# Kernel tuning notes

Measured on AMD Instinct MI355X. Metric: run time of the kernel, lower is better.

Reference implementation:

```python
import jax, jax.numpy as jnp
import numpy as np

# ---- Kymatio-style Morlet scattering filter bank (J=2, L=8, padded 40x40) ----
_CACHE = {}
_MP = 40  # 32 + 2*4 reflect padding, as in kymatio compute_padding for J=2

def _gabor(M, N, sigma, theta, xi, slant):
    R = np.array([[np.cos(theta), -np.sin(theta)], [np.sin(theta), np.cos(theta)]])
    D = np.array([[1.0, 0.0], [0.0, slant ** 2]])
    curv = R @ D @ R.T / (2.0 * sigma ** 2)
    xx, yy = np.mgrid[0:M, 0:N]
    gab = np.zeros((M, N), np.complex128)
    for ex in range(-2, 3):  # periodize over 5x5 shifts
        for ey in range(-2, 3):
            xg = xx + ex * M
            yg = yy + ey * N
            arg = -(curv[0, 0] * xg * xg + (curv[0, 1] + curv[1, 0]) * xg * yg + curv[1, 1] * yg * yg) \
                  + 1j * (xg * xi * np.cos(theta) + yg * xi * np.sin(theta))
            gab += np.exp(arg)
    return gab / (2.0 * np.pi * sigma ** 2 / slant)

def _morlet(M, N, sigma, theta, xi, slant):
    wv = _gabor(M, N, sigma, theta, xi, slant)
    env = _gabor(M, N, sigma, theta, 0.0, slant)
    return wv - (wv.sum() / env.sum()) * env  # zero-mean Morlet

def _periodize(v, res):
    k = 2 ** res
    Mv, Nv = v.shape
    return v.reshape(k, Mv // k, k, Nv // k).mean(axis=(0, 2))

def _filters():
    if _CACHE:
        return _CACHE
    Mp = _MP
    phi = np.real(np.fft.fft2(_gabor(Mp, Mp, 0.8 * 2 ** 2, 0.0, 0.0, 1.0)))
    psis = {}
    for j in range(2):
        bank = []
        for t in range(8):
            theta = (3 - t) * np.pi / 8.0  # kymatio angle convention (L=8)
            bank.append(np.real(np.fft.fft2(_morlet(Mp, Mp, 0.8 * 2 ** j, theta, 3.0 * np.pi / 4.0 / 2 ** j, 0.5))))
        psis[j] = np.stack(bank)
    _CACHE['phi0'] = jnp.asarray(phi, jnp.float32)
    _CACHE['phi1'] = jnp.asarray(_periodize(phi, 1), jnp.float32)
    _CACHE['psi0'] = jnp.asarray(psis[0], jnp.float32)      # (8,40,40) j=0 at res 0
    _CACHE['psi1_r0'] = jnp.asarray(psis[1], jnp.float32)   # (8,40,40) j=1 at res 0
    return _CACHE

def _unpad_sub(y_real, k):
    # fourier lowpass output -> spatial subsample by k, then unpad 1-pixel border
    return y_real[..., ::k, ::k][..., 1:-1, 1:-1]

def _scatter(x):
    F = _filters()
    xp = jnp.pad(x, ((0, 0), (0, 0), (4, 4), (4, 4)), mode='reflect')  # (B,3,40,40)
    xf = jnp.fft.fft2(xp)
    def lowpass(u, phi, k):
        return _unpad_sub(jnp.fft.ifft2(jnp.fft.fft2(u) * phi).real, k)
    # order 0
    S0 = _unpad_sub(jnp.fft.ifft2(xf * F['phi0']).real, 4)[:, :, None]            # (B,3,1,8,8)
    # order 1, j1 = 0 (stays at res 0)
    U1a = jnp.abs(jnp.fft.ifft2(xf[:, :, None] * F['psi0']))                       # (B,3,8,40,40)
    S1a = lowpass(U1a, F['phi0'], 4)                                               # (B,3,8,8,8)
    # order 1, j1 = 1 (subsample by 2)
    U1b = jnp.abs(jnp.fft.ifft2(xf[:, :, None] * F['psi1_r0'])[..., ::2, ::2])     # (B,3,8,20,20)
    S1b = lowpass(U1b, F['phi1'], 2)                                               # (B,3,8,8,8)
    # order 2, j1=0 -> j2=1
    U2 = jnp.abs(jnp.fft.ifft2(jnp.fft.fft2(U1a)[:, :, :, None] * F['psi1_r0'])[..., ::2, ::2])  # (B,3,8,8,20,20)
    S2 = lowpass(U2, F['phi1'], 2).reshape(x.shape[0], 3, 64, 8, 8)
    return jnp.concatenate([S0, S1a, S1b, S2], axis=2)  # (B,3,81,8,8)

def _toeplitz_mult(G, H, v):
    # ToeplitzLike, corner=False -> f=(0,0): y = sum_i L(g_i) (L(h_i)^T v)
    # L(.) lower-triangular Toeplitz; done via length-2n FFT conv / correlation
    n = v.shape[-1]
    Lf = 2 * n
    Hf = jnp.fft.rfft(H, Lf)          # (r, F)
    Gf = jnp.fft.rfft(G, Lf)          # (r, F)
    Vf = jnp.fft.rfft(v, Lf)          # (B, F)
    T = jnp.fft.irfft(jnp.conj(Hf)[:, None, :] * Vf[None], Lf)[..., :n]   # (r,B,n) = L(h_i)^T v
    Tf = jnp.fft.rfft(T, Lf)
    y = jnp.fft.irfft(jnp.einsum('rf,rbf->bf', Gf, Tf), Lf)[..., :n]       # sum_i L(g_i) t_i
    return y

def setup_inputs() -> dict:
    key = jax.random.key(0)
    ks = jax.random.split(key, 5)
    B, n, r = 128, 3 * 81 * 8 * 8, 4
    x = jax.random.normal(ks[0], (B, 3, 32, 32), jnp.float32)
    gamma = jnp.ones((n,), jnp.float32)
    beta = jnp.zeros((n,), jnp.float32)
    G = jax.random.normal(ks[3], (r, n), jnp.float32) / np.float32(np.sqrt(n))
    H = jax.random.normal(ks[4], (r, n), jnp.float32) / np.float32(np.sqrt(n))
    return {"x": x, "gamma": gamma, "beta": beta, "G": G, "H": H}

def reference(x, gamma, beta, G, H):
    S = _scatter(x)                                   # (B,3,81,8,8)
    f = S.reshape(S.shape[0], -1)                     # (B, 15552)
    mu = f.mean(axis=0)
    var = f.var(axis=0)                               # biased var, training-mode BN
    f = (f - mu) / jnp.sqrt(var + 1e-5) * gamma + beta
    f = jax.nn.relu(f)
    y = _toeplitz_mult(G, H, f)
    return y[..., :10]
```

## Files before the change

kernel.cpp:

```cpp
#include <hip/hip_runtime.h>
#include <math.h>

#define NTHR 256

__device__ __forceinline__ int reflect32(int v) {
  if (v < 0) v = -v;
  if (v > 31) v = 62 - v;
  return v;
}

__device__ __forceinline__ void init_tw(float2* tw, int N, int tid) {
  for (int j = tid; j < N; j += NTHR) {
    float s, c;
    sincosf(-2.0f * (float)M_PI * (float)j / (float)N, &s, &c);
    tw[j] = make_float2(c, s);
  }
}

template<int N, int LD, int NK, bool INV, int B, int AS>
__device__ __forceinline__ void dftB_rows(const float2* __restrict__ io,
                                          float2* __restrict__ tmp,
                                          const float2* __restrict__ tw, int tid) {
  constexpr int G = N / NK;
  constexpr int UNITS = B * N * G;
  for (int u = tid; u < UNITS; u += NTHR) {
    const int a = u / (N * G);
    const int rem = u - a * (N * G);
    const int r = rem / G, kg = rem - G * r;
    float xr[NK], xi[NK], ar[NK], ai[NK];
#pragma unroll
    for (int j = 0; j < NK; ++j) {
      float2 w = tw[kg * NK + j];
      xr[j] = w.x; xi[j] = INV ? -w.y : w.y;
    }
    const float2* row = io + a * AS + r * LD;
    float2 v = row[N - 1];
#pragma unroll
    for (int j = 0; j < NK; ++j) { ar[j] = v.x; ai[j] = v.y; }
#pragma unroll 2
    for (int cc = N - 2; cc >= 0; --cc) {
      v = row[cc];
#pragma unroll
      for (int j = 0; j < NK; ++j) {
        float nr = fmaf(ar[j], xr[j], fmaf(-ai[j], xi[j], v.x));
        float ni = fmaf(ar[j], xi[j], fmaf(ai[j], xr[j], v.y));
        ar[j] = nr; ai[j] = ni;
      }
    }
    float2* orow = tmp + a * AS + r * LD + kg * NK;
#pragma unroll
    for (int j = 0; j < NK; ++j) orow[j] = make_float2(ar[j], ai[j]);
  }
}

template<int N, int LD, int NK, bool INV, int B, int AS>
__device__ __forceinline__ void dftB_cols(const float2* __restrict__ tmp,
                                          float2* __restrict__ io,
                                          const float2* __restrict__ tw, int tid) {
  constexpr int G = N / NK;
  constexpr int UNITS = B * N * G;
  for (int u = tid; u < UNITS; u += NTHR) {
    const int a = u / (N * G);
    const int rem = u - a * (N * G);
    const int k1g = rem / N, k2 = rem - N * k1g;
    float xr[NK], xi[NK], ar[NK], ai[NK];
#pragma unroll
    for (int j = 0; j < NK; ++j) {
      float2 w = tw[k1g * NK + j];
      xr[j] = w.x; xi[j] = INV ? -w.y : w.y;
    }
    const float2* col = tmp + a * AS + k2;
    float2 v = col[(N - 1) * LD];
#pragma unroll
    for (int j = 0; j < NK; ++j) { ar[j] = v.x; ai[j] = v.y; }
#pragma unroll 2
    for (int r = N - 2; r >= 0; --r) {
      v = col[r * LD];
#pragma unroll
      for (int j = 0; j < NK; ++j) {
        float nr = fmaf(ar[j], xr[j], fmaf(-ai[j], xi[j], v.x));
        float ni = fmaf(ar[j], xi[j], fmaf(ai[j], xr[j], v.y));
        ar[j] = nr; ai[j] = ni;
      }
    }
    constexpr float scale = INV ? (1.f / (float)(N * N)) : 1.f;
#pragma unroll
    for (int j = 0; j < NK; ++j)
      io[a * AS + (k1g * NK + j) * LD + k2] = make_float2(ar[j] * scale, ai[j] * scale);
  }
}

template<int N, int LD, int NK, bool INV, int B, int AS>
__device__ __forceinline__ void dft2dB(float2* io, float2* tmp, const float2* tw, int tid) {
  dftB_rows<N, LD, NK, INV, B, AS>(io, tmp, tw, tid);
  __syncthreads();
  dftB_cols<N, LD, NK, INV, B, AS>(tmp, io, tw, tid);
  __syncthreads();
}

template<int NK, int KH>
__device__ __forceinline__ void rdft40_rows(const float2* __restrict__ io,
                                            float2* __restrict__ tmp,
                                            const float2* __restrict__ tw, int tid) {
  constexpr int G = KH / NK;
  constexpr int UNITS = 40 * G;
  if (tid < UNITS) {
    const int r = tid / G, kg = tid - G * r;
    float xr[NK], xi[NK], ar[NK], ai[NK];
#pragma unroll
    for (int j = 0; j < NK; ++j) { float2 w = tw[kg * NK + j]; xr[j] = w.x; xi[j] = w.y; }
    const float2* row = io + r * 41;
    float v = row[39].x;
#pragma unroll
    for (int j = 0; j < NK; ++j) { ar[j] = v; ai[j] = 0.f; }
#pragma unroll 2
    for (int cc = 38; cc >= 0; --cc) {
      v = row[cc].x;
#pragma unroll
      for (int j = 0; j < NK; ++j) {
        float nr = fmaf(ar[j], xr[j], fmaf(-ai[j], xi[j], v));
        float ni = fmaf(ar[j], xi[j], ai[j] * xr[j]);
        ar[j] = nr; ai[j] = ni;
      }
    }
    float2* orow = tmp + r * 41 + kg * NK;
#pragma unroll
    for (int j = 0; j < NK; ++j) orow[j] = make_float2(ar[j], ai[j]);
  }
}

template<int NK, int KH>
__device__ __forceinline__ void dft40_colsK(const float2* __restrict__ tmp,
                                            float2* __restrict__ io,
                                            const float2* __restrict__ tw, int tid) {
  constexpr int G = 40 / NK;
  constexpr int UNITS = KH * G;
  if (tid < UNITS) {
    const int k1g = tid / KH, k2 = tid - KH * k1g;
    float xr[NK], xi[NK], ar[NK], ai[NK];
#pragma unroll
    for (int j = 0; j < NK; ++j) { float2 w = tw[k1g * NK + j]; xr[j] = w.x; xi[j] = w.y; }
    const float2* col = tmp + k2;
    float2 v = col[39 * 41];
#pragma unroll
    for (int j = 0; j < NK; ++j) { ar[j] = v.x; ai[j] = v.y; }
#pragma unroll 2
    for (int r = 38; r >= 0; --r) {
      v = col[r * 41];
#pragma unroll
      for (int j = 0; j < NK; ++j) {
        float nr = fmaf(ar[j], xr[j], fmaf(-ai[j], xi[j], v.x));
        float ni = fmaf(ar[j], xi[j], fmaf(ai[j], xr[j], v.y));
        ar[j] = nr; ai[j] = ni;
      }
    }
#pragma unroll
    for (int j = 0; j < NK; ++j)
      io[(k1g * NK + j) * 41 + k2] = make_float2(ar[j], ai[j]);
  }
}

__device__ __forceinline__ void mirror40(float2* __restrict__ A, int tid) {
  for (int o = tid; o < 760; o += NTHR) {
    int d = o / 40;
    int k2 = 21 + d, k1 = o - 40 * d;
    float2 v = A[((40 - k1) % 40) * 41 + (40 - k2)];
    A[k1 * 41 + k2] = make_float2(v.x, -v.y);
  }
}

__global__ __launch_bounds__(NTHR) void k_filters(float* __restrict__ filt) {
  const int fid = blockIdx.x;
  const int tid = threadIdx.x;

  __shared__ float2 WV[40 * 41];
  __shared__ float  EV[1600];
  __shared__ float2 T[40 * 41];
  __shared__ float2 tw40[40];
  __shared__ float  sred[3][4];
  __shared__ float  Kc[2];

  double sigma, theta, xi, slant; int morlet; int outOff;
  if (fid == 0)      { sigma = 3.2; theta = 0.0; xi = 0.0;                  slant = 1.0; morlet = 0; outOff = 0; }
  else if (fid <= 8) { int t = fid - 1; sigma = 0.8; theta = (3 - t) * M_PI / 8.0; xi = 3.0 * M_PI / 4.0; slant = 0.5; morlet = 1; outOff = 2000 + t * 1600; }
  else               { int t = fid - 9; sigma = 1.6; theta = (3 - t) * M_PI / 8.0; xi = 3.0 * M_PI / 8.0; slant = 0.5; morlet = 1; outOff = 14800 + t * 1600; }

  const double ctd = cos(theta), std_ = sin(theta);
  const double sl2 = slant * slant;
  const double inv2s = 1.0 / (2.0 * sigma * sigma);
  const float ca = (float)((ctd * ctd + sl2 * std_ * std_) * inv2s);
  const float cb = (float)((ctd * std_ * (1.0 - sl2)) * inv2s);
  const float cd = (float)((std_ * std_ + sl2 * ctd * ctd) * inv2s);
  const float rnorm = (float)(slant / (2.0 * M_PI * sigma * sigma));
  const float ct = (float)ctd, st = (float)std_;
  const float xif = (float)xi;

  float swr = 0.f, swi = 0.f, ser = 0.f;
  for (int o = tid; o < 1600; o += NTHR) {
    int xr = o / 40, yc = o - 40 * xr;
    float wr = 0.f, wi = 0.f, er = 0.f;
    for (int ex = -2; ex <= 2; ++ex) {
      for (int ey = -2; ey <= 2; ++ey) {
        float xg = (float)xr + ex * 40.f, yg = (float)yc + ey * 40.f;
        float e = expf(-(ca * xg * xg + 2.f * cb * xg * yg + cd * yg * yg));
        float ang = xif * (xg * ct + yg * st);
        float s, c;
        sincosf(ang, &s, &c);
        wr = fmaf(e, c, wr); wi = fmaf(e, s, wi); er += e;
      }
    }
    wr *= rnorm; wi *= rnorm; er *= rnorm;
    WV[xr * 41 + yc] = make_float2(wr, wi);
    EV[o] = er;
    swr += wr; swi += wi; ser += er;
  }
  for (int off = 32; off > 0; off >>= 1) {
    swr += __shfl_down(swr, off);
    swi += __shfl_down(swi, off);
    ser += __shfl_down(ser, off);
  }
  int lane = tid & 63, w = tid >> 6;
  if (lane == 0) { sred[0][w] = swr; sred[1][w] = swi; sred[2][w] = ser; }
  __syncthreads();
  if (tid == 0) {
    float A = 0, B = 0, C = 0;
    for (int i = 0; i < 4; ++i) { A += sred[0][i]; B += sred[1][i]; C += sred[2][i]; }
    Kc[0] = A / C; Kc[1] = B / C;
  }
  init_tw(tw40, 40, tid);
  __syncthreads();
  if (morlet) {
    for (int o = tid; o < 1600; o += NTHR) {
      int i = o / 40, j = o - 40 * i;
      float e = EV[o];
      WV[i * 41 + j].x -= Kc[0] * e;
      WV[i * 41 + j].y -= Kc[1] * e;
    }
  }
  __syncthreads();
  dft2dB<40, 41, 8, false, 1, 0>(WV, T, tw40, tid);
  for (int o = tid; o < 1600; o += NTHR) {
    int i = o / 40, j = o - 40 * i;
    filt[outOff + o] = WV[i * 41 + j].x;
  }
  if (fid == 0) {
    for (int q = tid; q < 400; q += NTHR) {
      int q1 = q / 20, q2 = q - 20 * q1;
      float v = 0.25f * (WV[q1 * 41 + q2].x + WV[(q1 + 20) * 41 + q2].x +
                         WV[q1 * 41 + (q2 + 20)].x + WV[(q1 + 20) * 41 + (q2 + 20)].x);
      filt[1600 + q] = v;
    }
  }
}

__global__ __launch_bounds__(NTHR) void k_fftx(const float* __restrict__ x,
                                               const float* __restrict__ filt,
                                               float2* __restrict__ xf_g,
                                               float* __restrict__ f) {
  const int bc = blockIdx.x;
  const int b = bc / 3, c = bc - 3 * b;
  const int tid = threadIdx.x;

  __shared__ float2 A[40 * 41], T[40 * 41];
  __shared__ float2 P[110], Q[110];
  __shared__ float2 tw40[40], tw10[10];

  init_tw(tw40, 40, tid);
  init_tw(tw10, 10, tid);

  const float* xb = x + (size_t)bc * 1024;
  for (int o = tid; o < 1600; o += NTHR) {
    int i = o / 40, j = o - 40 * i;
    int si = reflect32(i - 4), sj = reflect32(j - 4);
    A[i * 41 + j] = make_float2(xb[si * 32 + sj], 0.f);
  }
  __syncthreads();
  rdft40_rows<4, 24>(A, T, tw40, tid);
  __syncthreads();
  dft40_colsK<4, 24>(T, A, tw40, tid);
  __syncthreads();
  mirror40(A, tid);
  __syncthreads();
  for (int o = tid; o < 1600; o += NTHR) {
    int i = o / 40, j = o - 40 * i;
    xf_g[(size_t)bc * 1600 + o] = A[i * 41 + j];
  }

  const float* phi0 = filt;
  for (int q = tid; q < 100; q += NTHR) {
    int q1 = q / 10, q2 = q - 10 * q1;
    float re = 0.f, im = 0.f;
#pragma unroll
    for (int a2 = 0; a2 < 4; ++a2)
#pragma unroll
      for (int b2 = 0; b2 < 4; ++b2) {
        int i40 = q1 + 10 * a2, j40 = q2 + 10 * b2;
        float ph = phi0[i40 * 40 + j40];
        float2 v = A[i40 * 41 + j40];
        re = fmaf(v.x, ph, re); im = fmaf(v.y, ph, im);
      }
    P[q1 * 11 + q2] = make_float2(re * (1.f / 16.f), im * (1.f / 16.f));
  }
  __syncthreads();
  dft2dB<10, 11, 1, true, 1, 0>(P, Q, tw10, tid);
  float* fb = f + (size_t)b * 15552 + c * 5184;
  if (tid < 64) {
    int i = tid >> 3, j = tid & 7;
    fb[tid] = P[(i + 1) * 11 + (j + 1)].x;
  }
}

__global__ __launch_bounds__(NTHR) void k_main(const float2* __restrict__ xf_g,
                                               const float* __restrict__ filt,
                                               float* __restrict__ f) {
  const int blk = blockIdx.x;
  const int t = blk & 7;
  const int bc = blk >> 3;
  const int b = bc / 3, c = bc - 3 * b;
  const int tid = threadIdx.x;

  __shared__ float2 A[40 * 41];
  __shared__ float2 T[40 * 41];
  __shared__ float2 C[2 * 420];
  __shared__ float2 P[110], Q[110];
  __shared__ float2 tw40[40], tw20[20], tw10[10];

  const float* phi0 = filt;
  const float* phi1 = filt + 1600;
  const float* psi0 = filt + 2000;
  const float* psi1 = filt + 14800;

  init_tw(tw40, 40, tid);
  init_tw(tw20, 20, tid);
  init_tw(tw10, 10, tid);

  const float2* xf = xf_g + (size_t)bc * 1600;
  for (int o = tid; o < 1600; o += NTHR) {
    int i = o / 40, j = o - 40 * i;
    A[i * 41 + j] = xf[o];
  }
  __syncthreads();

  float* fb = f + (size_t)b * 15552 + c * 5184;

  const float* ps1t = psi1 + t * 1600;
  for (int q = tid; q < 400; q += NTHR) {
    int q1 = q / 20, q2 = q - 20 * q1;
    float re = 0.f, im = 0.f;
#pragma unroll
    for (int a2 = 0; a2 < 2; ++a2)
#pragma unroll
      for (int b2 = 0; b2 < 2; ++b2) {
        int i40 = q1 + 20 * a2, j40 = q2 + 20 * b2;
        float ph = ps1t[i40 * 40 + j40];
        float2 v = A[i40 * 41 + j40];
        re = fmaf(v.x, ph, re); im = fmaf(v.y, ph, im);
      }
    C[q1 * 21 + q2] = make_float2(re * 0.25f, im * 0.25f);
  }
  __syncthreads();
  dft2dB<20, 21, 2, true, 1, 420>(C, T, tw20, tid);
  for (int o = tid; o < 400; o += NTHR) {
    int i = o / 20, j = o - 20 * i;
    float2 z = C[i * 21 + j];
    C[i * 21 + j] = make_float2(sqrtf(fmaf(z.x, z.x, z.y * z.y)), 0.f);
  }
  __syncthreads();
  dft2dB<20, 21, 2, false, 1, 420>(C, T, tw20, tid);
  for (int q = tid; q < 100; q += NTHR) {
    int q1 = q / 10, q2 = q - 10 * q1;
    float re = 0.f, im = 0.f;
#pragma unroll
    for (int a2 = 0; a2 < 2; ++a2)
#pragma unroll
      for (int b2 = 0; b2 < 2; ++b2) {
        int i20 = q1 + 10 * a2, j20 = q2 + 10 * b2;
        float ph = phi1[i20 * 20 + j20];
        float2 v = C[i20 * 21 + j20];
        re = fmaf(v.x, ph, re); im = fmaf(v.y, ph, im);
      }
    Q[q1 * 11 + q2] = make_float2(re * 0.25f, im * 0.25f);
  }

  const float* ps0 = psi0 + t * 1600;
  for (int o = tid; o < 1600; o += NTHR) {
    int i = o / 40, j = o - 40 * i;
    float p = ps0[o];
    float2 v = A[i * 41 + j];
    A[i * 41 + j] = make_float2(v.x * p, v.y * p);
  }
  __syncthreads();
  dft2dB<40, 41, 8, true, 1, 0>(A, T, tw40, tid);
  for (int o = tid; o < 1600; o += NTHR) {
    int i = o / 40, j = o - 40 * i;
    float2 z = A[i * 41 + j];
    A[i * 41 + j] = make_float2(sqrtf(fmaf(z.x, z.x, z.y * z.y)), 0.f);
  }
  __syncthreads();
  rdft40_rows<4, 24>(A, T, tw40, tid);
  __syncthreads();
  dft40_colsK<4, 24>(T, A, tw40, tid);
  __syncthreads();
  mirror40(A, tid);
  __syncthreads();

  for (int q = tid; q < 100; q += NTHR) {
    int q1 = q / 10, q2 = q - 10 * q1;
    float re = 0.f, im = 0.f;
#pragma unroll
    for (int a2 = 0; a2 < 4; ++a2)
#pragma unroll
      for (int b2 = 0; b2 < 4; ++b2) {
        int i40 = q1 + 10 * a2, j40 = q2 + 10 * b2;
        float ph = phi0[i40 * 40 + j40];
        float2 v = A[i40 * 41 + j40];
        re = fmaf(v.x, ph, re); im = fmaf(v.y, ph, im);
      }
    float2 qb = Q[q1 * 11 + q2];
    P[q1 * 11 + q2] = make_float2(re * (1.f / 16.f) - qb.y, im * (1.f / 16.f) + qb.x);
  }
  __syncthreads();
  dft2dB<10, 11, 1, true, 1, 0>(P, C, tw10, tid);
  if (tid < 64) {
    int i = tid >> 3, j = tid & 7;
    float2 v = P[(i + 1) * 11 + (j + 1)];
    fb[(1 + t) * 64 + tid] = v.x;
    fb[(9 + t) * 64 + tid] = v.y;
  }

  for (int p = 0; p < 4; ++p) {
    const float* pa = psi1 + (2 * p) * 1600;
    const float* pb = psi1 + (2 * p + 1) * 1600;
    __syncthreads();
    for (int q = tid; q < 800; q += NTHR) {
      int a = (q >= 400) ? 1 : 0;
      int qq = q - 400 * a;
      const float* ps = a ? pb : pa;
      int q1 = qq / 20, q2 = qq - 20 * q1;
      float re = 0.f, im = 0.f;
#pragma unroll
      for (int a2 = 0; a2 < 2; ++a2)
#pragma unroll
        for (int b2 = 0; b2 < 2; ++b2) {
          int i40 = q1 + 20 * a2, j40 = q2 + 20 * b2;
          float ph = ps[i40 * 40 + j40];
          float2 v = A[i40 * 41 + j40];
          re = fmaf(v.x, ph, re); im = fmaf(v.y, ph, im);
        }
      C[a * 420 + q1 * 21 + q2] = make_float2(re * 0.25f, im * 0.25f);
    }
    __syncthreads();
    dft2dB<20, 21, 2, true, 2, 420>(C, T, tw20, tid);
    for (int o = tid; o < 400; o += NTHR) {
      int i = o / 20, j = o - 20 * i;
      int idx = i * 21 + j;
      float2 z0 = C[idx], z1 = C[420 + idx];
      C[idx] = make_float2(sqrtf(fmaf(z0.x, z0.x, z0.y * z0.y)),
                           sqrtf(fmaf(z1.x, z1.x, z1.y * z1.y)));
    }
    __syncthreads();
    dft2dB<20, 21, 2, false, 1, 420>(C, T, tw20, tid);
    for (int q = tid; q < 100; q += NTHR) {
      int q1 = q / 10, q2 = q - 10 * q1;
      float re = 0.f, im = 0.f;
#pragma unroll
      for (int a2 = 0; a2 < 2; ++a2)
#pragma unroll
        for (int b2 = 0; b2 < 2; ++b2) {
          int i20 = q1 + 10 * a2, j20 = q2 + 10 * b2;
          float ph = phi1[i20 * 20 + j20];
          float2 v = C[i20 * 21 + j20];
          re = fmaf(v.x, ph, re); im = fmaf(v.y, ph, im);
        }
      P[q1 * 11 + q2] = make_float2(re * 0.25f, im * 0.25f);
    }
    __syncthreads();
    dft2dB<10, 11, 1, true, 1, 0>(P, C + 420, tw10, tid);
    if (tid < 64) {
      int i = tid >> 3, j = tid & 7;
      float2 v = P[(i + 1) * 11 + (j + 1)];
      fb[(17 + t * 8 + 2 * p) * 64 + tid] = v.x;
      fb[(17 + t * 8 + 2 * p + 1) * 64 + tid] = v.y;
    }
  }
}

__global__ __launch_bounds__(NTHR) void k_bn(const float* __restrict__ f,
                                             float* __restrict__ mu,
                                             float* __restrict__ rstd) {
  int col = blockIdx.x * NTHR + threadIdx.x;
  if (col >= 15552) return;
  double s = 0.0, s2 = 0.0;
  for (int b = 0; b < 128; ++b) {
    float v = f[(size_t)b * 15552 + col];
    s += v; s2 += (double)v * v;
  }
  double m = s / 128.0;
  double var = s2 / 128.0 - m * m;
  mu[col] = (float)m;
  rstd[col] = (float)(1.0 / sqrt(var + 1e-5));
}

__global__ __launch_bounds__(NTHR) void k_norm(const float* __restrict__ f,
                                               const float* __restrict__ mu,
                                               const float* __restrict__ rstd,
                                               const float* __restrict__ gamma,
                                               const float* __restrict__ beta,
                                               float* __restrict__ g) {
  size_t i = (size_t)blockIdx.x * NTHR + threadIdx.x;
  if (i >= (size_t)128 * 15552) return;
  int col = (int)(i % 15552);
  float v = (f[i] - mu[col]) * rstd[col] * gamma[col] + beta[col];
  g[i] = v > 0.f ? v : 0.f;
}

__global__ __launch_bounds__(NTHR) void k_out(const float* __restrict__ g,
                                              const float* __restrict__ Gm,
                                              const float* __restrict__ Hm,
                                              float* __restrict__ out) {
  const int b = blockIdx.x;
  const int tid = threadIdx.x;
  const float* gb = g + (size_t)b * 15552;

  float acc[40];
#pragma unroll
  for (int i = 0; i < 40; ++i) acc[i] = 0.f;

  for (int j = tid; j < 15552; j += NTHR) {
    float h[4];
#pragma unroll
    for (int r = 0; r < 4; ++r) h[r] = Hm[r * 15552 + j];
#pragma unroll
    for (int m = 0; m < 10; ++m) {
      int jm = j + m;
      float gv = (jm < 15552) ? gb[jm] : 0.f;
#pragma unroll
      for (int r = 0; r < 4; ++r) acc[r * 10 + m] += h[r] * gv;
    }
  }
#pragma unroll
  for (int i = 0; i < 40; ++i)
    for (int off = 32; off > 0; off >>= 1)
      acc[i] += __shfl_down(acc[i], off);

  __shared__ float red[4][40];
  __shared__ float Tm[40];
  int lane = tid & 63, w = tid >> 6;
  if (lane == 0) {
#pragma unroll
    for (int i = 0; i < 40; ++i) red[w][i] = acc[i];
  }
  __syncthreads();
  if (tid < 40) Tm[tid] = red[0][tid] + red[1][tid] + red[2][tid] + red[3][tid];
  __syncthreads();
  if (tid < 10) {
    float y = 0.f;
    for (int r = 0; r < 4; ++r)
      for (int m = 0; m <= tid; ++m)
        y += Gm[r * 15552 + (tid - m)] * Tm[r * 10 + m];
    out[b * 10 + tid] = y;
  }
}

extern "C" void kernel_launch(void* const* d_in, const int* in_sizes, int n_in,
                              void* d_out, int out_size, void* d_ws, size_t ws_size,
                              hipStream_t stream) {
  (void)in_sizes; (void)n_in; (void)out_size; (void)ws_size;
  const float* x     = (const float*)d_in[0];
  const float* gamma = (const float*)d_in[1];
  const float* beta  = (const float*)d_in[2];
  const float* G     = (const float*)d_in[3];
  const float* H     = (const float*)d_in[4];
  float* out = (float*)d_out;

  float* ws   = (float*)d_ws;
  float* filt = ws;
  float* xf   = filt + 27600;
  float* f    = xf + 1228800;
  float* g    = f + 1990656;
  float* mu   = g + 1990656;
  float* rstd = mu + 15552;

  k_filters<<<17, NTHR, 0, stream>>>(filt);
  k_fftx<<<384, NTHR, 0, stream>>>(x, filt, (float2*)xf, f);
  k_main<<<3072, NTHR, 0, stream>>>((const float2*)xf, filt, f);
  k_bn<<<61, NTHR, 0, stream>>>(f, mu, rstd);
  k_norm<<<7776, NTHR, 0, stream>>>(f, mu, rstd, gamma, beta, g);
  k_out<<<128, NTHR, 0, stream>>>(g, G, H, out);
}
```

Measured before the change: 393.3 us.

## Use radix-8x5 FFT for 40-point transforms, pre-permute filters, fuse BN into output

Replaces the direct 40-point DFTs (real-input rows plus mirror) with a two-stage 8x5 Cooley-Tukey factorisation with twiddles. This cuts the per-image FFT arithmetic in the main and input kernels. The filter kernel now stores lowpass filters pre-scaled and permuted so the periodization sums can use float4 loads. The four second-order inverse 10x10 transforms are batched into one pass, and the phi1 lowpass result is folded directly into the combined P buffer. The normalize+ReLU kernel is fused into the Toeplitz output kernel via a shared-memory tile, removing the intermediate g buffer and one launch.

```diff
diff --git a/kernel.cpp b/kernel.cpp
--- a/kernel.cpp
+++ b/kernel.cpp
@@ -98,75 +98,150 @@
   __syncthreads();
 }
 
-template<int NK, int KH>
-__device__ __forceinline__ void rdft40_rows(const float2* __restrict__ io,
-                                            float2* __restrict__ tmp,
-                                            const float2* __restrict__ tw, int tid) {
-  constexpr int G = KH / NK;
-  constexpr int UNITS = 40 * G;
-  if (tid < UNITS) {
-    const int r = tid / G, kg = tid - G * r;
-    float xr[NK], xi[NK], ar[NK], ai[NK];
-#pragma unroll
-    for (int j = 0; j < NK; ++j) { float2 w = tw[kg * NK + j]; xr[j] = w.x; xi[j] = w.y; }
-    const float2* row = io + r * 41;
-    float v = row[39].x;
-#pragma unroll
-    for (int j = 0; j < NK; ++j) { ar[j] = v; ai[j] = 0.f; }
-#pragma unroll 2
-    for (int cc = 38; cc >= 0; --cc) {
-      v = row[cc].x;
-#pragma unroll
-      for (int j = 0; j < NK; ++j) {
-        float nr = fmaf(ar[j], xr[j], fmaf(-ai[j], xi[j], v));
-        float ni = fmaf(ar[j], xi[j], ai[j] * xr[j]);
-        ar[j] = nr; ai[j] = ni;
-      }
-    }
-    float2* orow = tmp + r * 41 + kg * NK;
-#pragma unroll
-    for (int j = 0; j < NK; ++j) orow[j] = make_float2(ar[j], ai[j]);
-  }
-}
-
-template<int NK, int KH>
-__device__ __forceinline__ void dft40_colsK(const float2* __restrict__ tmp,
-                                            float2* __restrict__ io,
-                                            const float2* __restrict__ tw, int tid) {
-  constexpr int G = 40 / NK;
-  constexpr int UNITS = KH * G;
-  if (tid < UNITS) {
-    const int k1g = tid / KH, k2 = tid - KH * k1g;
-    float xr[NK], xi[NK], ar[NK], ai[NK];
-#pragma unroll
-    for (int j = 0; j < NK; ++j) { float2 w = tw[k1g * NK + j]; xr[j] = w.x; xi[j] = w.y; }
-    const float2* col = tmp + k2;
-    float2 v = col[39 * 41];
-#pragma unroll
-    for (int j = 0; j < NK; ++j) { ar[j] = v.x; ai[j] = v.y; }
-#pragma unroll 2
-    for (int r = 38; r >= 0; --r) {
-      v = col[r * 41];
-#pragma unroll
-      for (int j = 0; j < NK; ++j) {
-        float nr = fmaf(ar[j], xr[j], fmaf(-ai[j], xi[j], v.x));
-        float ni = fmaf(ar[j], xi[j], fmaf(ai[j], xr[j], v.y));
-        ar[j] = nr; ai[j] = ni;
-      }
-    }
-#pragma unroll
-    for (int j = 0; j < NK; ++j)
-      io[(k1g * NK + j) * 41 + k2] = make_float2(ar[j], ai[j]);
-  }
-}
-
-__device__ __forceinline__ void mirror40(float2* __restrict__ A, int tid) {
-  for (int o = tid; o < 760; o += NTHR) {
-    int d = o / 40;
-    int k2 = 21 + d, k1 = o - 40 * d;
-    float2 v = A[((40 - k1) % 40) * 41 + (40 - k2)];
-    A[k1 * 41 + k2] = make_float2(v.x, -v.y);
-  }
+template<bool INV>
+__device__ __forceinline__ void r40_rowsA(const float2* __restrict__ io, float2* __restrict__ T,
+                                          const float2* __restrict__ tw, int tid) {
+  if (tid < 200) {
+    const int r = tid / 5, n2 = tid - 5 * r;
+    const float2* base = io + r * 41 + n2;
+    float xr[8], xi[8], ar[8], ai[8];
+#pragma unroll
+    for (int k1 = 0; k1 < 8; ++k1) {
+      float2 w = tw[5 * k1];
+      xr[k1] = w.x; xi[k1] = INV ? -w.y : w.y;
+    }
+    float2 v = base[35];
+#pragma unroll
+    for (int k1 = 0; k1 < 8; ++k1) { ar[k1] = v.x; ai[k1] = v.y; }
+#pragma unroll
+    for (int n1 = 6; n1 >= 0; --n1) {
+      v = base[5 * n1];
+#pragma unroll
+      for (int k1 = 0; k1 < 8; ++k1) {
+        float nr = fmaf(ar[k1], xr[k1], fmaf(-ai[k1], xi[k1], v.x));
+        float ni = fmaf(ar[k1], xi[k1], fmaf(ai[k1], xr[k1], v.y));
+        ar[k1] = nr; ai[k1] = ni;
+      }
+    }
+    float2* o = T + r * 41 + n2 * 8;
+#pragma unroll
+    for (int k1 = 0; k1 < 8; ++k1) {
+      float2 w = tw[n2 * k1];
+      float wy = INV ? -w.y : w.y;
+      o[k1] = make_float2(ar[k1] * w.x - ai[k1] * wy, ar[k1] * wy + ai[k1] * w.x);
+    }
+  }
+}
+
+template<bool INV>
+__device__ __forceinline__ void r40_rowsB(const float2* __restrict__ T, float2* __restrict__ io,
+                                          const float2* __restrict__ tw, int tid) {
+  for (int u = tid; u < 320; u += NTHR) {
+    const int r = u >> 3, k1 = u & 7;
+    const float2* base = T + r * 41 + k1;
+    float xr[5], xi[5], ar[5], ai[5];
+#pragma unroll
+    for (int k2 = 0; k2 < 5; ++k2) {
+      float2 w = tw[8 * k2];
+      xr[k2] = w.x; xi[k2] = INV ? -w.y : w.y;
+    }
+    float2 v = base[32];
+#pragma unroll
+    for (int k2 = 0; k2 < 5; ++k2) { ar[k2] = v.x; ai[k2] = v.y; }
+#pragma unroll
+    for (int n2 = 3; n2 >= 0; --n2) {
+      v = base[n2 * 8];
+#pragma unroll
+      for (int k2 = 0; k2 < 5; ++k2) {
+        float nr = fmaf(ar[k2], xr[k2], fmaf(-ai[k2], xi[k2], v.x));
+        float ni = fmaf(ar[k2], xi[k2], fmaf(ai[k2], xr[k2], v.y));
+        ar[k2] = nr; ai[k2] = ni;
+      }
+    }
+    float2* o = io + r * 41 + k1;
+#pragma unroll
+    for (int k2 = 0; k2 < 5; ++k2) o[8 * k2] = make_float2(ar[k2], ai[k2]);
+  }
+}
+
+template<bool INV>
+__device__ __forceinline__ void r40_colsA(const float2* __restrict__ io, float2* __restrict__ T,
+                                          const float2* __restrict__ tw, int tid) {
+  if (tid < 200) {
+    const int n2 = tid / 40, c = tid - 40 * n2;
+    const float2* base = io + n2 * 41 + c;
+    float xr[8], xi[8], ar[8], ai[8];
+#pragma unroll
+    for (int k1 = 0; k1 < 8; ++k1) {
+      float2 w = tw[5 * k1];
+      xr[k1] = w.x; xi[k1] = INV ? -w.y : w.y;
+    }
+    float2 v = base[35 * 41];
+#pragma unroll
+    for (int k1 = 0; k1 < 8; ++k1) { ar[k1] = v.x; ai[k1] = v.y; }
+#pragma unroll
+    for (int n1 = 6; n1 >= 0; --n1) {
+      v = base[5 * n1 * 41];
+#pragma unroll
+      for (int k1 = 0; k1 < 8; ++k1) {
+        float nr = fmaf(ar[k1], xr[k1], fmaf(-ai[k1], xi[k1], v.x));
+        float ni = fmaf(ar[k1], xi[k1], fmaf(ai[k1], xr[k1], v.y));
+        ar[k1] = nr; ai[k1] = ni;
+      }
+    }
+    float2* o = T + n2 * 8 * 41 + c;
+#pragma unroll
+    for (int k1 = 0; k1 < 8; ++k1) {
+      float2 w = tw[n2 * k1];
+      float wy = INV ? -w.y : w.y;
+      o[k1 * 41] = make_float2(ar[k1] * w.x - ai[k1] * wy, ar[k1] * wy + ai[k1] * w.x);
+    }
+  }
+}
+
+template<bool INV>
+__device__ __forceinline__ void r40_colsB(const float2* __restrict__ T, float2* __restrict__ io,
+                                          const float2* __restrict__ tw, int tid) {
+  constexpr float scale = INV ? (1.f / 1600.f) : 1.f;
+  for (int u = tid; u < 320; u += NTHR) {
+    const int k1 = u / 40, c = u - 40 * k1;
+    const float2* base = T + k1 * 41 + c;
+    float xr[5], xi[5], ar[5], ai[5];
+#pragma unroll
+    for (int k2 = 0; k2 < 5; ++k2) {
+      float2 w = tw[8 * k2];
+      xr[k2] = w.x; xi[k2] = INV ? -w.y : w.y;
+    }
+    float2 v = base[4 * 8 * 41];
+#pragma unroll
+    for (int k2 = 0; k2 < 5; ++k2) { ar[k2] = v.x; ai[k2] = v.y; }
+#pragma unroll
+    for (int n2 = 3; n2 >= 0; --n2) {
+      v = base[n2 * 8 * 41];
+#pragma unroll
+      for (int k2 = 0; k2 < 5; ++k2) {
+        float nr = fmaf(ar[k2], xr[k2], fmaf(-ai[k2], xi[k2], v.x));
+        float ni = fmaf(ar[k2], xi[k2], fmaf(ai[k2], xr[k2], v.y));
+        ar[k2] = nr; ai[k2] = ni;
+      }
+    }
+    float2* o = io + k1 * 41 + c;
+#pragma unroll
+    for (int k2 = 0; k2 < 5; ++k2)
+      o[8 * k2 * 41] = make_float2(ar[k2] * scale, ai[k2] * scale);
+  }
+}
+
+template<bool INV>
+__device__ __forceinline__ void radix40(float2* io, float2* T, const float2* tw, int tid) {
+  r40_rowsA<INV>(io, T, tw, tid);
+  __syncthreads();
+  r40_rowsB<INV>(T, io, tw, tid);
+  __syncthreads();
+  r40_colsA<INV>(io, T, tw, tid);
+  __syncthreads();
+  r40_colsB<INV>(T, io, tw, tid);
+  __syncthreads();
 }
 
 __global__ __launch_bounds__(NTHR) void k_filters(float* __restrict__ filt) {
@@ -180,10 +255,10 @@
   __shared__ float  sred[3][4];
   __shared__ float  Kc[2];
 
-  double sigma, theta, xi, slant; int morlet; int outOff;
-  if (fid == 0)      { sigma = 3.2; theta = 0.0; xi = 0.0;                  slant = 1.0; morlet = 0; outOff = 0; }
-  else if (fid <= 8) { int t = fid - 1; sigma = 0.8; theta = (3 - t) * M_PI / 8.0; xi = 3.0 * M_PI / 4.0; slant = 0.5; morlet = 1; outOff = 2000 + t * 1600; }
-  else               { int t = fid - 9; sigma = 1.6; theta = (3 - t) * M_PI / 8.0; xi = 3.0 * M_PI / 8.0; slant = 0.5; morlet = 1; outOff = 14800 + t * 1600; }
+  double sigma, theta, xi, slant; int morlet;
+  if (fid == 0)      { sigma = 3.2; theta = 0.0; xi = 0.0;                  slant = 1.0; morlet = 0; }
+  else if (fid <= 8) { int t = fid - 1; sigma = 0.8; theta = (3 - t) * M_PI / 8.0; xi = 3.0 * M_PI / 4.0; slant = 0.5; morlet = 1; }
+  else               { int t = fid - 9; sigma = 1.6; theta = (3 - t) * M_PI / 8.0; xi = 3.0 * M_PI / 8.0; slant = 0.5; morlet = 1; }
 
   const double ctd = cos(theta), std_ = sin(theta);
   const double sl2 = slant * slant;
@@ -239,16 +314,42 @@
   }
   __syncthreads();
   dft2dB<40, 41, 8, false, 1, 0>(WV, T, tw40, tid);
-  for (int o = tid; o < 1600; o += NTHR) {
-    int i = o / 40, j = o - 40 * i;
-    filt[outOff + o] = WV[i * 41 + j].x;
-  }
+
   if (fid == 0) {
+    for (int o = tid; o < 1600; o += NTHR) {
+      int q = o >> 4, j = o & 15;
+      int q1 = q / 10, q2 = q - 10 * q1;
+      int a2 = j >> 2, b2 = j & 3;
+      filt[o] = WV[(q1 + 10 * a2) * 41 + (q2 + 10 * b2)].x * (1.f / 16.f);
+    }
+    for (int m = tid; m < 400; m += NTHR) {
+      int m1 = m / 20, m2 = m - 20 * m1;
+      EV[m] = 0.25f * (WV[m1 * 41 + m2].x + WV[(m1 + 20) * 41 + m2].x +
+                       WV[m1 * 41 + m2 + 20].x + WV[(m1 + 20) * 41 + m2 + 20].x);
+    }
+    __syncthreads();
+    for (int o = tid; o < 400; o += NTHR) {
+      int q = o >> 2, j = o & 3;
+      int q1 = q / 10, q2 = q - 10 * q1;
+      int a2 = j >> 1, b2 = j & 1;
+      filt[1600 + o] = EV[(q1 + 10 * a2) * 20 + (q2 + 10 * b2)] * 0.25f;
+    }
+  } else if (fid <= 8) {
+    int t = fid - 1;
+    for (int o = tid; o < 1600; o += NTHR) {
+      int i = o / 40, j = o - 40 * i;
+      filt[2000 + t * 1600 + o] = WV[i * 41 + j].x;
+    }
+  } else {
+    int t = fid - 9;
     for (int q = tid; q < 400; q += NTHR) {
       int q1 = q / 20, q2 = q - 20 * q1;
-      float v = 0.25f * (WV[q1 * 41 + q2].x + WV[(q1 + 20) * 41 + q2].x +
-                         WV[q1 * 41 + (q2 + 20)].x + WV[(q1 + 20) * 41 + (q2 + 20)].x);
-      filt[1600 + q] = v;
+      int base = q1 * 41 + q2;
+      float* o = filt + 14800 + t * 1600 + q * 4;
+      o[0] = WV[base].x * 0.25f;
+      o[1] = WV[base + 20].x * 0.25f;
+      o[2] = WV[base + 820].x * 0.25f;
+      o[3] = WV[base + 840].x * 0.25f;
     }
   }
 }
@@ -262,7 +363,7 @@
   const int tid = threadIdx.x;
 
   __shared__ float2 A[40 * 41], T[40 * 41];
-  __shared__ float2 P[110], Q[110];
+  __shared__ float2 P[110];
   __shared__ float2 tw40[40], tw10[10];
 
   init_tw(tw40, 40, tid);
@@ -275,34 +376,31 @@
     A[i * 41 + j] = make_float2(xb[si * 32 + sj], 0.f);
   }
   __syncthreads();
-  rdft40_rows<4, 24>(A, T, tw40, tid);
-  __syncthreads();
-  dft40_colsK<4, 24>(T, A, tw40, tid);
-  __syncthreads();
-  mirror40(A, tid);
-  __syncthreads();
+  radix40<false>(A, T, tw40, tid);
   for (int o = tid; o < 1600; o += NTHR) {
     int i = o / 40, j = o - 40 * i;
     xf_g[(size_t)bc * 1600 + o] = A[i * 41 + j];
   }
 
-  const float* phi0 = filt;
+  const float4* ph0f4 = (const float4*)filt;
   for (int q = tid; q < 100; q += NTHR) {
     int q1 = q / 10, q2 = q - 10 * q1;
+    int base = q1 * 41 + q2;
     float re = 0.f, im = 0.f;
 #pragma unroll
-    for (int a2 = 0; a2 < 4; ++a2)
-#pragma unroll
-      for (int b2 = 0; b2 < 4; ++b2) {
-        int i40 = q1 + 10 * a2, j40 = q2 + 10 * b2;
-        float ph = phi0[i40 * 40 + j40];
-        float2 v = A[i40 * 41 + j40];
-        re = fmaf(v.x, ph, re); im = fmaf(v.y, ph, im);
-      }
-    P[q1 * 11 + q2] = make_float2(re * (1.f / 16.f), im * (1.f / 16.f));
-  }
-  __syncthreads();
-  dft2dB<10, 11, 1, true, 1, 0>(P, Q, tw10, tid);
+    for (int a2 = 0; a2 < 4; ++a2) {
+      float4 pf = ph0f4[q * 4 + a2];
+      float2 v0 = A[base + a2 * 410];
+      float2 v1 = A[base + a2 * 410 + 10];
+      float2 v2 = A[base + a2 * 410 + 20];
+      float2 v3 = A[base + a2 * 410 + 30];
+      re = fmaf(v0.x, pf.x, fmaf(v1.x, pf.y, fmaf(v2.x, pf.z, fmaf(v3.x, pf.w, re))));
+      im = fmaf(v0.y, pf.x, fmaf(v1.y, pf.y, fmaf(v2.y, pf.z, fmaf(v3.y, pf.w, im))));
+    }
+    P[q1 * 11 + q2] = make_float2(re, im);
+  }
+  __syncthreads();
+  dft2dB<10, 11, 1, true, 1, 0>(P, T, tw10, tid);
   float* fb = f + (size_t)b * 15552 + c * 5184;
   if (tid < 64) {
     int i = tid >> 3, j = tid & 7;
@@ -322,13 +420,14 @@
   __shared__ float2 A[40 * 41];
   __shared__ float2 T[40 * 41];
   __shared__ float2 C[2 * 420];
-  __shared__ float2 P[110], Q[110];
+  __shared__ float2 P[110];
+  __shared__ float2 P4[4 * 110];
   __shared__ float2 tw40[40], tw20[20], tw10[10];
 
-  const float* phi0 = filt;
-  const float* phi1 = filt + 1600;
-  const float* psi0 = filt + 2000;
-  const float* psi1 = filt + 14800;
+  const float4* ph0f4 = (const float4*)filt;
+  const float4* ph1f4 = (const float4*)(filt + 1600);
+  const float*  psi0  = filt + 2000;
+  const float4* ps1f4 = (const float4*)(filt + 14800);
 
   init_tw(tw40, 40, tid);
   init_tw(tw20, 20, tid);
@@ -343,20 +442,14 @@
 
   float* fb = f + (size_t)b * 15552 + c * 5184;
 
-  const float* ps1t = psi1 + t * 1600;
   for (int q = tid; q < 400; q += NTHR) {
     int q1 = q / 20, q2 = q - 20 * q1;
-    float re = 0.f, im = 0.f;
-#pragma unroll
-    for (int a2 = 0; a2 < 2; ++a2)
-#pragma unroll
-      for (int b2 = 0; b2 < 2; ++b2) {
-        int i40 = q1 + 20 * a2, j40 = q2 + 20 * b2;
-        float ph = ps1t[i40 * 40 + j40];
-        float2 v = A[i40 * 41 + j40];
-        re = fmaf(v.x, ph, re); im = fmaf(v.y, ph, im);
-      }
-    C[q1 * 21 + q2] = make_float2(re * 0.25f, im * 0.25f);
+    int base = q1 * 41 + q2;
+    float4 pf = ps1f4[t * 400 + q];
+    float2 v0 = A[base], v1 = A[base + 20], v2 = A[base + 820], v3 = A[base + 840];
+    float re = fmaf(v0.x, pf.x, fmaf(v1.x, pf.y, fmaf(v2.x, pf.z, v3.x * pf.w)));
+    float im = fmaf(v0.y, pf.x, fmaf(v1.y, pf.y, fmaf(v2.y, pf.z, v3.y * pf.w)));
+    C[q1 * 21 + q2] = make_float2(re, im);
   }
   __syncthreads();
   dft2dB<20, 21, 2, true, 1, 420>(C, T, tw20, tid);
@@ -369,20 +462,16 @@
   dft2dB<20, 21, 2, false, 1, 420>(C, T, tw20, tid);
   for (int q = tid; q < 100; q += NTHR) {
     int q1 = q / 10, q2 = q - 10 * q1;
-    float re = 0.f, im = 0.f;
-#pragma unroll
-    for (int a2 = 0; a2 < 2; ++a2)
-#pragma unroll
-      for (int b2 = 0; b2 < 2; ++b2) {
-        int i20 = q1 + 10 * a2, j20 = q2 + 10 * b2;
-        float ph = phi1[i20 * 20 + j20];
-        float2 v = C[i20 * 21 + j20];
-        re = fmaf(v.x, ph, re); im = fmaf(v.y, ph, im);
-      }
-    Q[q1 * 11 + q2] = make_float2(re * 0.25f, im * 0.25f);
+    int base = q1 * 21 + q2;
+    float4 pf = ph1f4[q];
+    float2 v0 = C[base], v1 = C[base + 10], v2 = C[base + 210], v3 = C[base + 220];
+    float re = fmaf(v0.x, pf.x, fmaf(v1.x, pf.y, fmaf(v2.x, pf.z, v3.x * pf.w)));
+    float im = fmaf(v0.y, pf.x, fmaf(v1.y, pf.y, fmaf(v2.y, pf.z, v3.y * pf.w)));
+    P[q1 * 11 + q2] = make_float2(-im, re);
   }
 
   const float* ps0 = psi0 + t * 1600;
+  __syncthreads();
   for (int o = tid; o < 1600; o += NTHR) {
     int i = o / 40, j = o - 40 * i;
     float p = ps0[o];
@@ -390,37 +479,34 @@
     A[i * 41 + j] = make_float2(v.x * p, v.y * p);
   }
   __syncthreads();
-  dft2dB<40, 41, 8, true, 1, 0>(A, T, tw40, tid);
+  radix40<true>(A, T, tw40, tid);
   for (int o = tid; o < 1600; o += NTHR) {
     int i = o / 40, j = o - 40 * i;
     float2 z = A[i * 41 + j];
     A[i * 41 + j] = make_float2(sqrtf(fmaf(z.x, z.x, z.y * z.y)), 0.f);
   }
   __syncthreads();
-  rdft40_rows<4, 24>(A, T, tw40, tid);
-  __syncthreads();
-  dft40_colsK<4, 24>(T, A, tw40, tid);
-  __syncthreads();
-  mirror40(A, tid);
-  __syncthreads();
+  radix40<false>(A, T, tw40, tid);
 
   for (int q = tid; q < 100; q += NTHR) {
     int q1 = q / 10, q2 = q - 10 * q1;
+    int base = q1 * 41 + q2;
     float re = 0.f, im = 0.f;
 #pragma unroll
-    for (int a2 = 0; a2 < 4; ++a2)
-#pragma unroll
-      for (int b2 = 0; b2 < 4; ++b2) {
-        int i40 = q1 + 10 * a2, j40 = q2 + 10 * b2;
-        float ph = phi0[i40 * 40 + j40];
-        float2 v = A[i40 * 41 + j40];
-        re = fmaf(v.x, ph, re); im = fmaf(v.y, ph, im);
-      }
-    float2 qb = Q[q1 * 11 + q2];
-    P[q1 * 11 + q2] = make_float2(re * (1.f / 16.f) - qb.y, im * (1.f / 16.f) + qb.x);
-  }
-  __syncthreads();
-  dft2dB<10, 11, 1, true, 1, 0>(P, C, tw10, tid);
+    for (int a2 = 0; a2 < 4; ++a2) {
+      float4 pf = ph0f4[q * 4 + a2];
+      float2 v0 = A[base + a2 * 410];
+      float2 v1 = A[base + a2 * 410 + 10];
+      float2 v2 = A[base + a2 * 410 + 20];
+      float2 v3 = A[base + a2 * 410 + 30];
+      re = fmaf(v0.x, pf.x, fmaf(v1.x, pf.y, fmaf(v2.x, pf.z, fmaf(v3.x, pf.w, re))));
+      im = fmaf(v0.y, pf.x, fmaf(v1.y, pf.y, fmaf(v2.y, pf.z, fmaf(v3.y, pf.w, im))));
+    }
+    float2 prev = P[q1 * 11 + q2];
+    P[q1 * 11 + q2] = make_float2(prev.x + re, prev.y + im);
+  }
+  __syncthreads();
+  dft2dB<10, 11, 1, true, 1, 0>(P, T, tw10, tid);
   if (tid < 64) {
     int i = tid >> 3, j = tid & 7;
     float2 v = P[(i + 1) * 11 + (j + 1)];
@@ -429,25 +515,17 @@
   }
 
   for (int p = 0; p < 4; ++p) {
-    const float* pa = psi1 + (2 * p) * 1600;
-    const float* pb = psi1 + (2 * p + 1) * 1600;
     __syncthreads();
-    for (int q = tid; q < 800; q += NTHR) {
-      int a = (q >= 400) ? 1 : 0;
-      int qq = q - 400 * a;
-      const float* ps = a ? pb : pa;
-      int q1 = qq / 20, q2 = qq - 20 * q1;
-      float re = 0.f, im = 0.f;
-#pragma unroll
-      for (int a2 = 0; a2 < 2; ++a2)
-#pragma unroll
-        for (int b2 = 0; b2 < 2; ++b2) {
-          int i40 = q1 + 20 * a2, j40 = q2 + 20 * b2;
-          float ph = ps[i40 * 40 + j40];
-          float2 v = A[i40 * 41 + j40];
-          re = fmaf(v.x, ph, re); im = fmaf(v.y, ph, im);
-        }
-      C[a * 420 + q1 * 21 + q2] = make_float2(re * 0.25f, im * 0.25f);
+    for (int u = tid; u < 800; u += NTHR) {
+      int a = (u >= 400) ? 1 : 0;
+      int q = u - 400 * a;
+      int q1 = q / 20, q2 = q - 20 * q1;
+      int base = q1 * 41 + q2;
+      float4 pf = ps1f4[(2 * p + a) * 400 + q];
+      float2 v0 = A[base], v1 = A[base + 20], v2 = A[base + 820], v3 = A[base + 840];
+      float re = fmaf(v0.x, pf.x, fmaf(v1.x, pf.y, fmaf(v2.x, pf.z, v3.x * pf.w)));
+      float im = fmaf(v0.y, pf.x, fmaf(v1.y, pf.y, fmaf(v2.y, pf.z, v3.y * pf.w)));
+      C[a * 420 + q1 * 21 + q2] = make_float2(re, im);
     }
     __syncthreads();
     dft2dB<20, 21, 2, true, 2, 420>(C, T, tw20, tid);
@@ -462,26 +540,22 @@
     dft2dB<20, 21, 2, false, 1, 420>(C, T, tw20, tid);
     for (int q = tid; q < 100; q += NTHR) {
       int q1 = q / 10, q2 = q - 10 * q1;
-      float re = 0.f, im = 0.f;
-#pragma unroll
-      for (int a2 = 0; a2 < 2; ++a2)
-#pragma unroll
-        for (int b2 = 0; b2 < 2; ++b2) {
-          int i20 = q1 + 10 * a2, j20 = q2 + 10 * b2;
-          float ph = phi1[i20 * 20 + j20];
-          float2 v = C[i20 * 21 + j20];
-          re = fmaf(v.x, ph, re); im = fmaf(v.y, ph, im);
-        }
-      P[q1 * 11 + q2] = make_float2(re * 0.25f, im * 0.25f);
-    }
-    __syncthreads();
-    dft2dB<10, 11, 1, true, 1, 0>(P, C + 420, tw10, tid);
-    if (tid < 64) {
-      int i = tid >> 3, j = tid & 7;
-      float2 v = P[(i + 1) * 11 + (j + 1)];
-      fb[(17 + t * 8 + 2 * p) * 64 + tid] = v.x;
-      fb[(17 + t * 8 + 2 * p + 1) * 64 + tid] = v.y;
-    }
+      int base = q1 * 21 + q2;
+      float4 pf = ph1f4[q];
+      float2 v0 = C[base], v1 = C[base + 10], v2 = C[base + 210], v3 = C[base + 220];
+      float re = fmaf(v0.x, pf.x, fmaf(v1.x, pf.y, fmaf(v2.x, pf.z, v3.x * pf.w)));
+      float im = fmaf(v0.y, pf.x, fmaf(v1.y, pf.y, fmaf(v2.y, pf.z, v3.y * pf.w)));
+      P4[p * 110 + q1 * 11 + q2] = make_float2(re, im);
+    }
+  }
+  __syncthreads();
+  dft2dB<10, 11, 1, true, 4, 110>(P4, T, tw10, tid);
+  {
+    int p = tid >> 6, o = tid & 63;
+    int i = o >> 3, j = o & 7;
+    float2 v = P4[p * 110 + (i + 1) * 11 + (j + 1)];
+    fb[(17 + t * 8 + 2 * p) * 64 + o] = v.x;
+    fb[(17 + t * 8 + 2 * p + 1) * 64 + o] = v.y;
   }
 }
 
@@ -501,42 +575,53 @@
   rstd[col] = (float)(1.0 / sqrt(var + 1e-5));
 }
 
-__global__ __launch_bounds__(NTHR) void k_norm(const float* __restrict__ f,
-                                               const float* __restrict__ mu,
-                                               const float* __restrict__ rstd,
-                                               const float* __restrict__ gamma,
-                                               const float* __restrict__ beta,
-                                               float* __restrict__ g) {
-  size_t i = (size_t)blockIdx.x * NTHR + threadIdx.x;
-  if (i >= (size_t)128 * 15552) return;
-  int col = (int)(i % 15552);
-  float v = (f[i] - mu[col]) * rstd[col] * gamma[col] + beta[col];
-  g[i] = v > 0.f ? v : 0.f;
-}
-
-__global__ __launch_bounds__(NTHR) void k_out(const float* __restrict__ g,
+__global__ __launch_bounds__(NTHR) void k_out(const float* __restrict__ f,
+                                              const float* __restrict__ mu,
+                                              const float* __restrict__ rstd,
+                                              const float* __restrict__ gamma,
+                                              const float* __restrict__ beta,
                                               const float* __restrict__ Gm,
                                               const float* __restrict__ Hm,
                                               float* __restrict__ out) {
   const int b = blockIdx.x;
   const int tid = threadIdx.x;
-  const float* gb = g + (size_t)b * 15552;
-
+  const float* fbp = f + (size_t)b * 15552;
+
+  __shared__ float sg[NTHR + 10];
   float acc[40];
 #pragma unroll
   for (int i = 0; i < 40; ++i) acc[i] = 0.f;
 
-  for (int j = tid; j < 15552; j += NTHR) {
-    float h[4];
-#pragma unroll
-    for (int r = 0; r < 4; ++r) h[r] = Hm[r * 15552 + j];
-#pragma unroll
-    for (int m = 0; m < 10; ++m) {
-      int jm = j + m;
-      float gv = (jm < 15552) ? gb[jm] : 0.f;
-#pragma unroll
-      for (int r = 0; r < 4; ++r) acc[r * 10 + m] += h[r] * gv;
-    }
+  for (int base = 0; base < 15552; base += NTHR) {
+    int j = base + tid;
+    float v = 0.f;
+    if (j < 15552) {
+      v = (fbp[j] - mu[j]) * rstd[j] * gamma[j] + beta[j];
+      v = v > 0.f ? v : 0.f;
+    }
+    sg[tid] = v;
+    if (tid < 10) {
+      int j2 = base + NTHR + tid;
+      float v2 = 0.f;
+      if (j2 < 15552) {
+        v2 = (fbp[j2] - mu[j2]) * rstd[j2] * gamma[j2] + beta[j2];
+        v2 = v2 > 0.f ? v2 : 0.f;
+      }
+      sg[NTHR + tid] = v2;
+    }
+    __syncthreads();
+    if (j < 15552) {
+      float h[4];
+#pragma unroll
+      for (int r = 0; r < 4; ++r) h[r] = Hm[r * 15552 + j];
+#pragma unroll
+      for (int m = 0; m < 10; ++m) {
+        float gv = sg[tid + m];
+#pragma unroll
+        for (int r = 0; r < 4; ++r) acc[r * 10 + m] = fmaf(h[r], gv, acc[r * 10 + m]);
+      }
+    }
+    __syncthreads();
   }
 #pragma unroll
   for (int i = 0; i < 40; ++i)
@@ -577,14 +662,12 @@
   float* filt = ws;
   float* xf   = filt + 27600;
   float* f    = xf + 1228800;
-  float* g    = f + 1990656;
-  float* mu   = g + 1990656;
+  float* mu   = f + 1990656;
   float* rstd = mu + 15552;
 
   k_filters<<<17, NTHR, 0, stream>>>(filt);
   k_fftx<<<384, NTHR, 0, stream>>>(x, filt, (float2*)xf, f);
   k_main<<<3072, NTHR, 0, stream>>>((const float2*)xf, filt, f);
   k_bn<<<61, NTHR, 0, stream>>>(f, mu, rstd);
-  k_norm<<<7776, NTHR, 0, stream>>>(f, mu, rstd, gamma, beta, g);
-  k_out<<<128, NTHR, 0, stream>>>(g, G, H, out);
-}
+  k_out<<<128, NTHR, 0, stream>>>(f, mu, rstd, gamma, beta, G, H, out);
+}
```

Result: faster. 382.1 us (-2.9%).
